# Kernel optimization log

Hardware: AMD Instinct MI355X
Metric: run time of the kernel (lower is better)

Reference implementation:

```python
import jax, jax.numpy as jnp
import numpy as np

DIM = 768
N_HEADS = 12
HEAD_DIM = DIM // N_HEADS
SCALE = HEAD_DIM ** (-0.5)


def setup_inputs() -> dict:
    key = jax.random.key(0)
    ks = jax.random.split(key, 5)
    B, N = 8, 1024
    x = jax.random.normal(ks[0], (B, N, DIM), dtype=jnp.float32)
    # parameters (fan-in scaled init)
    w_qkv = jax.random.normal(ks[1], (DIM, 3 * DIM), dtype=jnp.float32) / np.sqrt(DIM)
    b_qkv = jnp.zeros((3 * DIM,), dtype=jnp.float32)
    w_proj = jax.random.normal(ks[2], (DIM, DIM), dtype=jnp.float32) / np.sqrt(DIM)
    b_proj = jnp.zeros((DIM,), dtype=jnp.float32)
    return {"x": x, "w_qkv": w_qkv, "b_qkv": b_qkv, "w_proj": w_proj, "b_proj": b_proj}


def reference(x, w_qkv, b_qkv, w_proj, b_proj):
    B, N, D = x.shape
    qkv = x @ w_qkv + b_qkv                       # [B, N, 3D]
    qkv = qkv.reshape(B, N, 3, N_HEADS, HEAD_DIM)
    qkv = jnp.transpose(qkv, (2, 0, 3, 1, 4))     # [3, B, H, N, hd]
    q, k, v = qkv[0], qkv[1], qkv[2]
    attn = jax.nn.softmax(jnp.einsum('bhnd,bhmd->bhnm', q, k) * SCALE, axis=-1)
    wa = jnp.einsum('bhnm,bhmd->bhnd', attn, v)   # [B, H, N, hd]
    wa = jnp.transpose(wa, (0, 2, 1, 3)).reshape(B, N, D)
    return wa @ w_proj + b_proj
```

## Files before the change

### kernel.cpp

```cpp
#include <hip/hip_runtime.h>
#include <hip/hip_bf16.h>

#define DIM 768
#define NH  12
#define HD  64
#define B_  8
#define N_  1024

typedef short bf16x8 __attribute__((ext_vector_type(8)));
typedef float f32x4  __attribute__((ext_vector_type(4)));

__device__ __forceinline__ ushort f2b(float x) {
  union { __hip_bfloat16 h; ushort u; } cv;
  cv.h = __float2bfloat16(x);
  return cv.u;
}

#define GLDS16(gp, lp)                                                                 \
  __builtin_amdgcn_global_load_lds((const __attribute__((address_space(1))) void*)(gp),\
                                   (__attribute__((address_space(3))) void*)(lp),      \
                                   16, 0, 0)

__global__ __launch_bounds__(256) void cast_x_kernel(const float* __restrict__ src,
                                                     ushort* __restrict__ dst, int n4) {
  int idx = blockIdx.x * 256 + threadIdx.x;
  int stride = gridDim.x * 256;
  for (int i = idx; i < n4; i += stride) {
    float4 v = reinterpret_cast<const float4*>(src)[i];
    ushort4 o;
    o.x = f2b(v.x); o.y = f2b(v.y); o.z = f2b(v.z); o.w = f2b(v.w);
    reinterpret_cast<ushort4*>(dst)[i] = o;
  }
}

__global__ __launch_bounds__(256) void transpose_cast_kernel(const float* __restrict__ src,
                                                             ushort* __restrict__ dst,
                                                             int R, int C) {
  __shared__ float tile[32][33];
  const int tx = threadIdx.x & 31, ty = threadIdx.x >> 5;
  const int r0 = blockIdx.y * 32, c0 = blockIdx.x * 32;
  #pragma unroll
  for (int i = 0; i < 32; i += 8)
    tile[ty + i][tx] = src[(size_t)(r0 + ty + i) * C + c0 + tx];
  __syncthreads();
  #pragma unroll
  for (int i = 0; i < 32; i += 8)
    dst[(size_t)(c0 + ty + i) * R + r0 + tx] = f2b(tile[tx][ty + i]);
}

__device__ __forceinline__ void gemm128(const ushort* __restrict__ A,
                                        const ushort* __restrict__ Bt, const int K,
                                        const int rowA0, const int rowB0,
                                        ushort* sA, ushort* sB, f32x4 acc[4][4]) {
  const int tid  = threadIdx.x;
  const int lane = tid & 63;
  const int w    = tid >> 6;
  const int wr   = w >> 1, wc = w & 1;

  int srow[4], soff[4];
  #pragma unroll
  for (int p = 0; p < 4; ++p) {
    int L   = (w * 4 + p) * 1024 + lane * 16;
    int row = L >> 7;
    int cb  = L & 127;
    srow[p] = row;
    soff[p] = cb ^ ((row & 7) << 4);
  }

  const int nk = K >> 6;
  for (int kt = 0; kt < nk; ++kt) {
    __syncthreads();
    #pragma unroll
    for (int p = 0; p < 4; ++p) {
      const char* ga = (const char*)A  + ((size_t)(rowA0 + srow[p]) * K + kt * 64) * 2 + soff[p];
      GLDS16(ga, (char*)sA + (w * 4 + p) * 1024);
      const char* gb = (const char*)Bt + ((size_t)(rowB0 + srow[p]) * K + kt * 64) * 2 + soff[p];
      GLDS16(gb, (char*)sB + (w * 4 + p) * 1024);
    }
    asm volatile("s_waitcnt vmcnt(0)" ::: "memory");
    __syncthreads();

    #pragma unroll
    for (int kk = 0; kk < 2; ++kk) {
      bf16x8 af[4], bfr[4];
      #pragma unroll
      for (int mi = 0; mi < 4; ++mi) {
        int row = wr * 64 + mi * 16 + (lane & 15);
        int cb  = kk * 64 + ((lane >> 4) << 4);
        af[mi] = *(const bf16x8*)((const char*)sA + row * 128 + (cb ^ ((row & 7) << 4)));
      }
      #pragma unroll
      for (int ni = 0; ni < 4; ++ni) {
        int row = wc * 64 + ni * 16 + (lane & 15);
        int cb  = kk * 64 + ((lane >> 4) << 4);
        bfr[ni] = *(const bf16x8*)((const char*)sB + row * 128 + (cb ^ ((row & 7) << 4)));
      }
      #pragma unroll
      for (int mi = 0; mi < 4; ++mi)
        #pragma unroll
        for (int ni = 0; ni < 4; ++ni)
          acc[mi][ni] = __builtin_amdgcn_mfma_f32_16x16x32_bf16(af[mi], bfr[ni], acc[mi][ni], 0, 0, 0);
    }
  }
}

__global__ __launch_bounds__(256) void qkv_gemm_kernel(const ushort* __restrict__ xb,
                                                       const ushort* __restrict__ wqkvT,
                                                       const float* __restrict__ bqkv,
                                                       ushort* __restrict__ Qb,
                                                       ushort* __restrict__ Kb,
                                                       ushort* __restrict__ Vt) {
  __shared__ ushort sA[128 * 64], sB[128 * 64];
  const int nt = blockIdx.x % 18;
  const int mt = blockIdx.x / 18;
  const int tileM = mt * 128, tileC = nt * 128;

  f32x4 acc[4][4] = {};
  gemm128(xb, wqkvT, DIM, tileM, tileC, sA, sB, acc);

  const int lane = threadIdx.x & 63, w = threadIdx.x >> 6;
  const int wr = w >> 1, wc = w & 1;
  const int s  = tileC / DIM;
  const int b  = tileM >> 10;
  const int n0 = (tileM & 1023) + wr * 64;
  const int h  = ((tileC % DIM) + wc * 64) >> 6;
  const int bh = b * NH + h;

  #pragma unroll
  for (int ni = 0; ni < 4; ++ni) {
    const int d = ni * 16 + (lane & 15);
    const float bias = bqkv[tileC + wc * 64 + d];
    #pragma unroll
    for (int mi = 0; mi < 4; ++mi) {
      #pragma unroll
      for (int j = 0; j < 4; ++j) {
        const int n = n0 + mi * 16 + ((lane >> 4) << 2) + j;
        const float v = acc[mi][ni][j] + bias;
        if (s == 0)      Qb[((size_t)bh * N_ + n) * HD + d] = f2b(v * 0.125f);
        else if (s == 1) Kb[((size_t)bh * N_ + n) * HD + d] = f2b(v);
        else             Vt[((size_t)bh * HD + d) * N_ + n] = f2b(v);
      }
    }
  }
}

__global__ __launch_bounds__(256) void attn_kernel(const ushort* __restrict__ Qb,
                                                   const ushort* __restrict__ Kb,
                                                   const ushort* __restrict__ Vt,
                                                   ushort* __restrict__ AO) {
  __shared__ ushort P[4][32 * 72];
  const int bh = blockIdx.x >> 3;
  const int qt = blockIdx.x & 7;
  const int lane = threadIdx.x & 63, w = threadIdx.x >> 6;
  const int q0 = qt * 128 + w * 32;
  const ushort* Qh = Qb + (size_t)bh * N_ * HD;
  const ushort* Kh = Kb + (size_t)bh * N_ * HD;
  const ushort* Vh = Vt + (size_t)bh * HD * N_;
  ushort* pb = P[w];

  bf16x8 qf[2][2];
  #pragma unroll
  for (int i = 0; i < 2; ++i)
    #pragma unroll
    for (int kk = 0; kk < 2; ++kk)
      qf[i][kk] = *(const bf16x8*)&Qh[(q0 + i * 16 + (lane & 15)) * HD + kk * 32 + ((lane >> 4) << 3)];

  f32x4 oacc[2][4] = {};
  float mrun[8], ssum[8];
  #pragma unroll
  for (int im = 0; im < 8; ++im) { mrun[im] = -1e30f; ssum[im] = 0.f; }

  for (int t = 0; t < 16; ++t) {
    const int kv0 = t * 64;
    f32x4 sacc[2][4] = {};
    #pragma unroll
    for (int kk = 0; kk < 2; ++kk) {
      bf16x8 kf[4];
      #pragma unroll
      for (int nf = 0; nf < 4; ++nf)
        kf[nf] = *(const bf16x8*)&Kh[(kv0 + nf * 16 + (lane & 15)) * HD + kk * 32 + ((lane >> 4) << 3)];
      #pragma unroll
      for (int i = 0; i < 2; ++i)
        #pragma unroll
        for (int nf = 0; nf < 4; ++nf)
          sacc[i][nf] = __builtin_amdgcn_mfma_f32_16x16x32_bf16(qf[i][kk], kf[nf], sacc[i][nf], 0, 0, 0);
    }
    #pragma unroll
    for (int i = 0; i < 2; ++i) {
      #pragma unroll
      for (int r = 0; r < 4; ++r) {
        const int im = i * 4 + r;
        float tm = fmaxf(fmaxf(sacc[i][0][r], sacc[i][1][r]),
                         fmaxf(sacc[i][2][r], sacc[i][3][r]));
        #pragma unroll
        for (int d = 1; d < 16; d <<= 1) tm = fmaxf(tm, __shfl_xor(tm, d));
        const float nm   = fmaxf(mrun[im], tm);
        const float corr = __expf(mrun[im] - nm);
        mrun[im] = nm;
        float rs = 0.f;
        const int prow = (i * 16 + ((lane >> 4) << 2) + r) * 72 + (lane & 15);
        #pragma unroll
        for (int nf = 0; nf < 4; ++nf) {
          const float p = __expf(sacc[i][nf][r] - nm);
          rs += p;
          pb[prow + nf * 16] = f2b(p);
        }
        #pragma unroll
        for (int d = 1; d < 16; d <<= 1) rs += __shfl_xor(rs, d);
        ssum[im] = ssum[im] * corr + rs;
        #pragma unroll
        for (int df = 0; df < 4; ++df) oacc[i][df][r] *= corr;
      }
    }
    #pragma unroll
    for (int kk = 0; kk < 2; ++kk) {
      bf16x8 pa[2], vf[4];
      #pragma unroll
      for (int i = 0; i < 2; ++i)
        pa[i] = *(const bf16x8*)&pb[(i * 16 + (lane & 15)) * 72 + kk * 32 + ((lane >> 4) << 3)];
      #pragma unroll
      for (int df = 0; df < 4; ++df)
        vf[df] = *(const bf16x8*)&Vh[(df * 16 + (lane & 15)) * N_ + kv0 + kk * 32 + ((lane >> 4) << 3)];
      #pragma unroll
      for (int i = 0; i < 2; ++i)
        #pragma unroll
        for (int df = 0; df < 4; ++df)
          oacc[i][df] = __builtin_amdgcn_mfma_f32_16x16x32_bf16(pa[i], vf[df], oacc[i][df], 0, 0, 0);
    }
  }
  const int btok = (bh / NH) * N_;
  const int hcol = (bh % NH) * HD;
  float inv[8];
  #pragma unroll
  for (int im = 0; im < 8; ++im) inv[im] = 1.f / ssum[im];
  #pragma unroll
  for (int i = 0; i < 2; ++i)
    #pragma unroll
    for (int df = 0; df < 4; ++df) {
      const int col = hcol + df * 16 + (lane & 15);
      #pragma unroll
      for (int r = 0; r < 4; ++r) {
        const int row = btok + q0 + i * 16 + ((lane >> 4) << 2) + r;
        AO[(size_t)row * DIM + col] = f2b(oacc[i][df][r] * inv[i * 4 + r]);
      }
    }
}

__global__ __launch_bounds__(256) void proj_gemm_kernel(const ushort* __restrict__ AO,
                                                        const ushort* __restrict__ wprojT,
                                                        const float* __restrict__ bproj,
                                                        float* __restrict__ out) {
  __shared__ ushort sA[128 * 64], sB[128 * 64];
  const int nt = blockIdx.x % 6;
  const int mt = blockIdx.x / 6;
  f32x4 acc[4][4] = {};
  gemm128(AO, wprojT, DIM, mt * 128, nt * 128, sA, sB, acc);

  const int lane = threadIdx.x & 63, w = threadIdx.x >> 6;
  const int wr = w >> 1, wc = w & 1;
  #pragma unroll
  for (int ni = 0; ni < 4; ++ni) {
    const int col = nt * 128 + wc * 64 + ni * 16 + (lane & 15);
    const float bias = bproj[col];
    #pragma unroll
    for (int mi = 0; mi < 4; ++mi) {
      const int row = mt * 128 + wr * 64 + mi * 16 + ((lane >> 4) << 2);
      #pragma unroll
      for (int j = 0; j < 4; ++j)
        out[(size_t)(row + j) * DIM + col] = acc[mi][ni][j] + bias;
    }
  }
}

extern "C" void kernel_launch(void* const* d_in, const int* in_sizes, int n_in,
                              void* d_out, int out_size, void* d_ws, size_t ws_size,
                              hipStream_t stream) {
  const float* x      = (const float*)d_in[0];
  const float* w_qkv  = (const float*)d_in[1];
  const float* b_qkv  = (const float*)d_in[2];
  const float* w_proj = (const float*)d_in[3];
  const float* b_proj = (const float*)d_in[4];
  float* out = (float*)d_out;

  ushort* xb     = (ushort*)d_ws;
  ushort* wqkvT  = xb + 6291456;
  ushort* wprojT = wqkvT + 1769472;
  ushort* Qb     = wprojT + 589824;
  ushort* Kb     = Qb + 6291456;
  ushort* Vt     = Kb + 6291456;
  ushort* AO     = Vt + 6291456;
  (void)in_sizes; (void)n_in; (void)out_size; (void)ws_size;

  cast_x_kernel<<<2048, 256, 0, stream>>>(x, xb, 6291456 / 4);
  transpose_cast_kernel<<<dim3(2304 / 32, 768 / 32), 256, 0, stream>>>(w_qkv, wqkvT, DIM, 3 * DIM);
  transpose_cast_kernel<<<dim3(768 / 32, 768 / 32), 256, 0, stream>>>(w_proj, wprojT, DIM, DIM);
  qkv_gemm_kernel<<<64 * 18, 256, 0, stream>>>(xb, wqkvT, b_qkv, Qb, Kb, Vt);
  attn_kernel<<<96 * 8, 256, 0, stream>>>(Qb, Kb, Vt, AO);
  proj_gemm_kernel<<<64 * 6, 256, 0, stream>>>(AO, wprojT, b_proj, out);
}
```

Baseline: 278.1 us.

## Prefetch K fragments, use exp2 softmax with lazy rescaling, defer row-sum reduction

Folds log2(e) into the Q scale so the softmax uses exp2f, and skips the running-max rescale of the accumulators unless some row's new max exceeds the old one by more than a threshold. The per-row sum is kept per lane and shuffle-reduced once at the end instead of every tile. K fragments for the next tile are loaded into registers during the current tile's softmax, and s_setprio is raised around the MFMA blocks. The block index mapping is also swapped so query tiles of different heads run together. The lazy rescale lets exponents grow up to 2^5 before renormalising, which slightly changes the numerical behaviour, and the prefetch raises register pressure.

```diff
diff --git a/kernel.cpp b/kernel.cpp
--- a/kernel.cpp
+++ b/kernel.cpp
@@ -126,6 +126,8 @@
   const int h  = ((tileC % DIM) + wc * 64) >> 6;
   const int bh = b * NH + h;
 
+  const float QSCALE = 0.125f * 1.4426950408889634f;
+
   #pragma unroll
   for (int ni = 0; ni < 4; ++ni) {
     const int d = ni * 16 + (lane & 15);
@@ -136,7 +138,7 @@
       for (int j = 0; j < 4; ++j) {
         const int n = n0 + mi * 16 + ((lane >> 4) << 2) + j;
         const float v = acc[mi][ni][j] + bias;
-        if (s == 0)      Qb[((size_t)bh * N_ + n) * HD + d] = f2b(v * 0.125f);
+        if (s == 0)      Qb[((size_t)bh * N_ + n) * HD + d] = f2b(v * QSCALE);
         else if (s == 1) Kb[((size_t)bh * N_ + n) * HD + d] = f2b(v);
         else             Vt[((size_t)bh * HD + d) * N_ + n] = f2b(v);
       }
@@ -149,8 +151,8 @@
                                                    const ushort* __restrict__ Vt,
                                                    ushort* __restrict__ AO) {
   __shared__ ushort P[4][32 * 72];
-  const int bh = blockIdx.x >> 3;
-  const int qt = blockIdx.x & 7;
+  const int bh = blockIdx.x % 96;
+  const int qt = blockIdx.x / 96;
   const int lane = threadIdx.x & 63, w = threadIdx.x >> 6;
   const int q0 = qt * 128 + w * 32;
   const ushort* Qh = Qb + (size_t)bh * N_ * HD;
@@ -166,25 +168,39 @@
       qf[i][kk] = *(const bf16x8*)&Qh[(q0 + i * 16 + (lane & 15)) * HD + kk * 32 + ((lane >> 4) << 3)];
 
   f32x4 oacc[2][4] = {};
-  float mrun[8], ssum[8];
-  #pragma unroll
-  for (int im = 0; im < 8; ++im) { mrun[im] = -1e30f; ssum[im] = 0.f; }
+  float mrun[8], psum[8];
+  #pragma unroll
+  for (int im = 0; im < 8; ++im) { mrun[im] = -1e30f; psum[im] = 0.f; }
+
+  bf16x8 kf[2][4];
+  #pragma unroll
+  for (int kk = 0; kk < 2; ++kk)
+    #pragma unroll
+    for (int nf = 0; nf < 4; ++nf)
+      kf[kk][nf] = *(const bf16x8*)&Kh[(nf * 16 + (lane & 15)) * HD + kk * 32 + ((lane >> 4) << 3)];
 
   for (int t = 0; t < 16; ++t) {
     const int kv0 = t * 64;
     f32x4 sacc[2][4] = {};
-    #pragma unroll
-    for (int kk = 0; kk < 2; ++kk) {
-      bf16x8 kf[4];
-      #pragma unroll
-      for (int nf = 0; nf < 4; ++nf)
-        kf[nf] = *(const bf16x8*)&Kh[(kv0 + nf * 16 + (lane & 15)) * HD + kk * 32 + ((lane >> 4) << 3)];
+    __builtin_amdgcn_s_setprio(1);
+    #pragma unroll
+    for (int kk = 0; kk < 2; ++kk)
       #pragma unroll
       for (int i = 0; i < 2; ++i)
         #pragma unroll
         for (int nf = 0; nf < 4; ++nf)
-          sacc[i][nf] = __builtin_amdgcn_mfma_f32_16x16x32_bf16(qf[i][kk], kf[nf], sacc[i][nf], 0, 0, 0);
-    }
+          sacc[i][nf] = __builtin_amdgcn_mfma_f32_16x16x32_bf16(qf[i][kk], kf[kk][nf], sacc[i][nf], 0, 0, 0);
+    __builtin_amdgcn_s_setprio(0);
+
+    if (t < 15) {
+      const int kn = kv0 + 64;
+      #pragma unroll
+      for (int kk = 0; kk < 2; ++kk)
+        #pragma unroll
+        for (int nf = 0; nf < 4; ++nf)
+          kf[kk][nf] = *(const bf16x8*)&Kh[(kn + nf * 16 + (lane & 15)) * HD + kk * 32 + ((lane >> 4) << 3)];
+    }
+
     #pragma unroll
     for (int i = 0; i < 2; ++i) {
       #pragma unroll
@@ -194,45 +210,56 @@
                          fmaxf(sacc[i][2][r], sacc[i][3][r]));
         #pragma unroll
         for (int d = 1; d < 16; d <<= 1) tm = fmaxf(tm, __shfl_xor(tm, d));
-        const float nm   = fmaxf(mrun[im], tm);
-        const float corr = __expf(mrun[im] - nm);
-        mrun[im] = nm;
+        if (__any(tm > mrun[im] + 5.0f)) {
+          const float nm   = fmaxf(mrun[im], tm);
+          const float corr = exp2f(mrun[im] - nm);
+          mrun[im] = nm;
+          psum[im] *= corr;
+          #pragma unroll
+          for (int df = 0; df < 4; ++df) oacc[i][df][r] *= corr;
+        }
+        const float m = mrun[im];
+        const int prow = (i * 16 + ((lane >> 4) << 2) + r) * 72 + (lane & 15);
         float rs = 0.f;
-        const int prow = (i * 16 + ((lane >> 4) << 2) + r) * 72 + (lane & 15);
         #pragma unroll
         for (int nf = 0; nf < 4; ++nf) {
-          const float p = __expf(sacc[i][nf][r] - nm);
+          const float p = exp2f(sacc[i][nf][r] - m);
           rs += p;
           pb[prow + nf * 16] = f2b(p);
         }
-        #pragma unroll
-        for (int d = 1; d < 16; d <<= 1) rs += __shfl_xor(rs, d);
-        ssum[im] = ssum[im] * corr + rs;
-        #pragma unroll
-        for (int df = 0; df < 4; ++df) oacc[i][df][r] *= corr;
-      }
-    }
+        psum[im] += rs;
+      }
+    }
+
     #pragma unroll
     for (int kk = 0; kk < 2; ++kk) {
       bf16x8 pa[2], vf[4];
       #pragma unroll
+      for (int df = 0; df < 4; ++df)
+        vf[df] = *(const bf16x8*)&Vh[(df * 16 + (lane & 15)) * N_ + kv0 + kk * 32 + ((lane >> 4) << 3)];
+      #pragma unroll
       for (int i = 0; i < 2; ++i)
         pa[i] = *(const bf16x8*)&pb[(i * 16 + (lane & 15)) * 72 + kk * 32 + ((lane >> 4) << 3)];
-      #pragma unroll
-      for (int df = 0; df < 4; ++df)
-        vf[df] = *(const bf16x8*)&Vh[(df * 16 + (lane & 15)) * N_ + kv0 + kk * 32 + ((lane >> 4) << 3)];
+      __builtin_amdgcn_s_setprio(1);
       #pragma unroll
       for (int i = 0; i < 2; ++i)
         #pragma unroll
         for (int df = 0; df < 4; ++df)
           oacc[i][df] = __builtin_amdgcn_mfma_f32_16x16x32_bf16(pa[i], vf[df], oacc[i][df], 0, 0, 0);
-    }
+      __builtin_amdgcn_s_setprio(0);
+    }
+  }
+
+  float inv[8];
+  #pragma unroll
+  for (int im = 0; im < 8; ++im) {
+    float s = psum[im];
+    #pragma unroll
+    for (int d = 1; d < 16; d <<= 1) s += __shfl_xor(s, d);
+    inv[im] = 1.f / s;
   }
   const int btok = (bh / NH) * N_;
   const int hcol = (bh % NH) * HD;
-  float inv[8];
-  #pragma unroll
-  for (int im = 0; im < 8; ++im) inv[im] = 1.f / ssum[im];
   #pragma unroll
   for (int i = 0; i < 2; ++i)
     #pragma unroll
```

New measurement: 282.9 us. About the same (+1.7%).
